# Kernel optimization log

Measured on AMD Instinct MI355X. Metric: run time of the kernel, lower is better.

Reference implementation:

```python
import jax, jax.numpy as jnp
import numpy as np

INPUT_LENGTH = 4096
NUM_FEATURES = 10000
KERNEL_LENGTH = 9
NUM_KERNELS = 84
EPS = 1e-12


def _compute_dilations(input_length):
    # mirrors MiniRocketTransform._compute_dilations exactly
    max_dilation = (input_length - 1) // (KERNEL_LENGTH - 1)
    dilations = np.logspace(0, np.log10(max_dilation), num=NUM_KERNELS, base=2, dtype=int)
    return np.unique(dilations).tolist()

DILATIONS = _compute_dilations(INPUT_LENGTH)  # static python ints


def _generate_kernels(seed=42):
    # mirrors MiniRocketTransform._generate_kernels; kernels with sum==0 dropped
    rng = np.random.RandomState(seed)
    ks = []
    for _ in range(NUM_KERNELS):
        k = rng.choice([-1, 2], size=KERNEL_LENGTH, p=[2.0 / 3.0, 1.0 / 3.0])
        if k.sum() != 0:
            ks.append(k)
    return np.asarray(ks, dtype=np.float32)


def setup_inputs() -> dict:
    key = jax.random.key(0)
    x = jax.random.normal(key, (256, 1, INPUT_LENGTH), dtype=jnp.float32)
    kernels = jnp.asarray(_generate_kernels())  # (Kn, 9)
    return {"x": x, "kernels": kernels}


def reference(x, kernels):
    # x: (B, 1, L); kernels: (Kn, 9) of {-1, 2}
    B = x.shape[0]
    w = kernels[:, None, :]  # (Kn, 1, 9) OIH

    # zero-stuffed dilated kernel + padding=0 (len((1,1,K) tensor)//2 == 0)
    # is exactly a VALID conv with rhs_dilation=d.
    def conv(xv, wv, d):
        return jax.lax.conv_general_dilated(
            xv, wv, window_strides=(1,), padding='VALID', rhs_dilation=(d,))

    # biases computed ONCE from the first kernel / first dilation conv output
    conv0 = conv(x, w[:1], DILATIONS[0])  # (B, 1, L0)
    q = jnp.quantile(conv0, jnp.array([0.25, 0.5, 0.75], dtype=conv0.dtype), axis=2)  # (3, B, 1)
    biases = q.mean(axis=1).reshape(3)  # (3,)

    feats = []
    for d in DILATIONS:  # small static set (~6)
        c = conv(x, w, d)  # (B, Kn, Ld)
        # PPV: fraction of positions where conv output exceeds each bias
        ppv = (c[:, :, None, :] > biases[None, None, :, None]).astype(jnp.float32).mean(axis=3)  # (B, Kn, 3)
        feats.append(ppv)

    # feature order in torch: kernel-major, then dilation, then bias
    f = jnp.stack(feats, axis=2).reshape(B, -1)  # (B, Kn*Dn*3)
    out = jnp.zeros((B, NUM_FEATURES), dtype=jnp.float32).at[:, :f.shape[1]].set(f)
    # F.normalize(p=2, dim=-1, eps=1e-12)
    norm = jnp.maximum(jnp.linalg.norm(out, axis=-1, keepdims=True), EPS)
    return out / norm
```

## Files before the change

kernel.cpp:

```cpp
#include <hip/hip_runtime.h>
#include <stdint.h>

#define IN_LEN 4096
#define NFEAT  10000

__device__ __forceinline__ void count_gt_f32(unsigned& cnt, float thr, float val) {
  asm volatile("v_cmp_lt_f32 vcc, %1, %2\n\t"
               "v_addc_co_u32 %0, vcc, 0, %0, vcc"
               : "+v"(cnt)
               : "v"(thr), "v"(val)
               : "vcc");
}
__device__ __forceinline__ void count_le_u32(unsigned& cnt, unsigned mid, unsigned key) {
  asm volatile("v_cmp_ge_u32 vcc, %1, %2\n\t"
               "v_addc_co_u32 %0, vcc, 0, %0, vcc"
               : "+v"(cnt)
               : "v"(mid), "v"(key)
               : "vcc");
}

__device__ __forceinline__ unsigned key_of(float f) {
  unsigned u = __float_as_uint(f);
  return (u & 0x80000000u) ? ~u : (u | 0x80000000u);
}
__device__ __forceinline__ float key_inv(unsigned k) {
  unsigned u = (k & 0x80000000u) ? (k ^ 0x80000000u) : ~k;
  return __uint_as_float(u);
}

__global__ __launch_bounds__(256) void quant_kernel(const float* __restrict__ x,
                                                    const float* __restrict__ kern,
                                                    float* __restrict__ ws_q) {
  const int b = blockIdx.x, tid = threadIdx.x;
  __shared__ __align__(16) float xs[IN_LEN];
  __shared__ unsigned redc[2][3 * 4];

  const float4* xg = (const float4*)(x + (size_t)b * IN_LEN);
  float4* xs4 = (float4*)xs;
  for (int i = tid; i < IN_LEN / 4; i += 256) xs4[i] = xg[i];

  float w[9];
#pragma unroll
  for (int j = 0; j < 9; j++) w[j] = kern[j];
  __syncthreads();

  const int L = IN_LEN - 8;
  unsigned keys[16];
#pragma unroll
  for (int i = 0; i < 16; i++) {
    int t = tid + (i << 8);
    if (t < L) {
      float c = 0.f;
#pragma unroll
      for (int j = 0; j < 9; j++) c = fmaf(w[j], xs[t + j], c);
      keys[i] = key_of(c);
    } else {
      keys[i] = 0xFFFFFFFFu;
    }
  }

  const int targ[6] = {1021, 1022, 2043, 2044, 3065, 3066};
  unsigned lo[6], hi[6];
#pragma unroll
  for (int q = 0; q < 6; q++) { lo[q] = 0u; hi[q] = 0xFFFFFFFFu; }

  const int wave = tid >> 6, lane = tid & 63;
  for (int it = 0; it < 32; ++it) {
    const int buf = it & 1;
    unsigned mid[6], cnt[6];
#pragma unroll
    for (int q = 0; q < 6; q++) { mid[q] = lo[q] + ((hi[q] - lo[q]) >> 1); cnt[q] = 0u; }
#pragma unroll
    for (int i = 0; i < 16; i++)
#pragma unroll
      for (int q = 0; q < 6; q++) count_le_u32(cnt[q], mid[q], keys[i]);
    unsigned r[3];
#pragma unroll
    for (int q = 0; q < 3; q++) r[q] = cnt[2 * q] | (cnt[2 * q + 1] << 16);
#pragma unroll
    for (int q = 0; q < 3; q++) {
#pragma unroll
      for (int off = 32; off > 0; off >>= 1) r[q] += (unsigned)__shfl_xor((int)r[q], off);
    }
    if (lane == 0) {
#pragma unroll
      for (int q = 0; q < 3; q++) redc[buf][q * 4 + wave] = r[q];
    }
    __syncthreads();
#pragma unroll
    for (int q = 0; q < 3; q++) {
      unsigned tot = redc[buf][q * 4 + 0] + redc[buf][q * 4 + 1] +
                     redc[buf][q * 4 + 2] + redc[buf][q * 4 + 3];
      unsigned t0 = tot & 0xFFFFu, t1 = tot >> 16;
      if (t0 >= (unsigned)(targ[2 * q] + 1)) hi[2 * q] = mid[2 * q]; else lo[2 * q] = mid[2 * q] + 1;
      if (t1 >= (unsigned)(targ[2 * q + 1] + 1)) hi[2 * q + 1] = mid[2 * q + 1]; else lo[2 * q + 1] = mid[2 * q + 1] + 1;
    }
  }

  if (tid == 0) {
    float v[6];
#pragma unroll
    for (int q = 0; q < 6; q++) v[q] = key_inv(lo[q]);
    ws_q[b * 3 + 0] = v[0] + 0.75f * (v[1] - v[0]);
    ws_q[b * 3 + 1] = v[2] + 0.5f  * (v[3] - v[2]);
    ws_q[b * 3 + 2] = v[4] + 0.25f * (v[5] - v[4]);
  }
}

__global__ __launch_bounds__(256) void bias_kernel(const float* __restrict__ ws_q,
                                                   float* __restrict__ ws_bias, int B) {
  __shared__ float red[256];
  const int tid = threadIdx.x;
  for (int q = 0; q < 3; q++) {
    float v = 0.f;
    for (int i = tid; i < B; i += 256) v += ws_q[i * 3 + q];
    red[tid] = v;
    __syncthreads();
    for (int s = 128; s > 0; s >>= 1) {
      if (tid < s) red[tid] += red[tid + s];
      __syncthreads();
    }
    if (tid == 0) ws_bias[q] = red[0] / (float)B;
    __syncthreads();
  }
}

template <int D>
__device__ __forceinline__ void run_feat(const float* xs,
                                         const float* __restrict__ kern,
                                         float b0, float b1, float b2,
                                         float* __restrict__ out, int K, int b) {
  const int tid = threadIdx.x;
  const int wave = tid >> 6, lane = tid & 63;
  constexpr int L = IN_LEN - 8 * D;
  constexpr int NFULL = 31;
  constexpr int KT = 8;

  const int KPW = (K + 3) >> 2;
  const int kstart = wave * KPW;
  const int kend = (kstart + KPW < K) ? (kstart + KPW) : K;

  for (int k0 = kstart; k0 < kend; k0 += KT) {
    float w[KT][9];
#pragma unroll
    for (int kk = 0; kk < KT; kk++) {
      const int kidx = (k0 + kk < K) ? (k0 + kk) : (K - 1);
      const bool ok = (k0 + kk) < kend;
      const float* wp = kern + (size_t)kidx * 9;
#pragma unroll
      for (int j = 0; j < 9; j++) w[kk][j] = ok ? wp[j] : 0.f;
    }
    unsigned c0[KT], c1[KT], c2[KT];
#pragma unroll
    for (int kk = 0; kk < KT; kk++) { c0[kk] = 0u; c1[kk] = 0u; c2[kk] = 0u; }

#pragma unroll 1
    for (int p = 0; p < NFULL; ++p) {
      const int t = (p << 7) + lane;
      float tax[9], tay[9];
#pragma unroll
      for (int j = 0; j < 9; j++) {
        tax[j] = xs[t + j * D];
        tay[j] = xs[t + 64 + j * D];
      }
#pragma unroll
      for (int kk = 0; kk < KT; kk++) {
        float ca = 0.f, cb = 0.f;
#pragma unroll
        for (int j = 0; j < 9; j++) {
          ca = fmaf(w[kk][j], tax[j], ca);
          cb = fmaf(w[kk][j], tay[j], cb);
        }
        count_gt_f32(c0[kk], b0, ca); count_gt_f32(c0[kk], b0, cb);
        count_gt_f32(c1[kk], b1, ca); count_gt_f32(c1[kk], b1, cb);
        count_gt_f32(c2[kk], b2, ca); count_gt_f32(c2[kk], b2, cb);
      }
    }
    {
      const int t = (NFULL << 7) + lane;
      const bool v0 = t < L, v1 = (t + 64) < L;
      float tax[9], tay[9];
#pragma unroll
      for (int j = 0; j < 9; j++) {
        tax[j] = xs[t + j * D];
        tay[j] = xs[t + 64 + j * D];
      }
#pragma unroll
      for (int kk = 0; kk < KT; kk++) {
        float ca = 0.f, cb = 0.f;
#pragma unroll
        for (int j = 0; j < 9; j++) {
          ca = fmaf(w[kk][j], tax[j], ca);
          cb = fmaf(w[kk][j], tay[j], cb);
        }
        ca = v0 ? ca : -3.0e38f;
        cb = v1 ? cb : -3.0e38f;
        count_gt_f32(c0[kk], b0, ca); count_gt_f32(c0[kk], b0, cb);
        count_gt_f32(c1[kk], b1, ca); count_gt_f32(c1[kk], b1, cb);
        count_gt_f32(c2[kk], b2, ca); count_gt_f32(c2[kk], b2, cb);
      }
    }

#pragma unroll
    for (int kk = 0; kk < KT; kk++) {
      unsigned r0 = c0[kk] | (c2[kk] << 16);
      unsigned r1 = c1[kk];
#pragma unroll
      for (int off = 32; off > 0; off >>= 1) {
        r0 += (unsigned)__shfl_xor((int)r0, off);
        r1 += (unsigned)__shfl_xor((int)r1, off);
      }
      const int k = k0 + kk;
      if (lane == 0 && k < kend) {
        float* o = out + (size_t)b * NFEAT + (size_t)k * 18 + (D - 1) * 3;
        o[0] = (float)(r0 & 0xFFFFu) / (float)L;
        o[1] = (float)r1 / (float)L;
        o[2] = (float)(r0 >> 16) / (float)L;
      }
    }
  }
}

__global__ __launch_bounds__(256) void feat_kernel(const float* __restrict__ x,
                                                   const float* __restrict__ kern,
                                                   const float* __restrict__ ws_bias,
                                                   float* __restrict__ out, int K) {
  __shared__ __align__(16) float xs[IN_LEN + 48];
  const int b = blockIdx.y, tid = threadIdx.x;

  const float4* xg = (const float4*)(x + (size_t)b * IN_LEN);
  float4* xs4 = (float4*)xs;
  for (int i = tid; i < IN_LEN / 4; i += 256) xs4[i] = xg[i];
  if (tid < 48) xs[IN_LEN + tid] = 0.f;
  const float b0 = ws_bias[0], b1 = ws_bias[1], b2 = ws_bias[2];
  __syncthreads();

  switch (blockIdx.x) {
    case 0: run_feat<1>(xs, kern, b0, b1, b2, out, K, b); break;
    case 1: run_feat<2>(xs, kern, b0, b1, b2, out, K, b); break;
    case 2: run_feat<3>(xs, kern, b0, b1, b2, out, K, b); break;
    case 3: run_feat<4>(xs, kern, b0, b1, b2, out, K, b); break;
    case 4: run_feat<5>(xs, kern, b0, b1, b2, out, K, b); break;
    case 5: run_feat<6>(xs, kern, b0, b1, b2, out, K, b); break;
  }
}

__global__ __launch_bounds__(256) void norm_kernel(float* __restrict__ out, int F) {
  const int b = blockIdx.x, tid = threadIdx.x;
  __shared__ float red[256];
  float acc = 0.f;
  for (int i = tid; i < F; i += 256) {
    float v = out[(size_t)b * NFEAT + i];
    acc = fmaf(v, v, acc);
  }
  red[tid] = acc;
  __syncthreads();
  for (int s = 128; s > 0; s >>= 1) {
    if (tid < s) red[tid] += red[tid + s];
    __syncthreads();
  }
  const float inv = 1.0f / fmaxf(sqrtf(red[0]), 1e-12f);
  for (int i = tid; i < F; i += 256) out[(size_t)b * NFEAT + i] *= inv;
}

extern "C" void kernel_launch(void* const* d_in, const int* in_sizes, int n_in,
                              void* d_out, int out_size, void* d_ws, size_t ws_size,
                              hipStream_t stream) {
  const float* x = (const float*)d_in[0];
  const float* kern = (const float*)d_in[1];
  float* out = (float*)d_out;
  const int B = in_sizes[0] / IN_LEN;
  const int K = in_sizes[1] / 9;

  float* ws_q = (float*)d_ws;
  float* ws_bias = ws_q + B * 3;

  hipMemsetAsync(d_out, 0, (size_t)out_size * sizeof(float), stream);

  quant_kernel<<<B, 256, 0, stream>>>(x, kern, ws_q);
  bias_kernel<<<1, 256, 0, stream>>>(ws_q, ws_bias, B);
  dim3 g(6, B);
  feat_kernel<<<g, 256, 0, stream>>>(x, kern, ws_bias, out, K);
  norm_kernel<<<B, 256, 0, stream>>>(out, K * 18);
}
```

Baseline: 231.2 us.

## Fuse bias and norm into producer kernels via last-block atomics, bitmask counting

Merges the bias reduction into the quantile kernel and the L2 normalization into the feature kernel, using atomic last-block-done counters. This removes two launches and the full-output memset, since the norm pass now writes the zero padding itself. Threshold comparisons are packed into bitmasks with alignbit on the sign of (bias - conv) and counted with popcount, with K tile reduced from 8 to 6 and an occupancy hint added. The atomic counters need a small workspace memset each call, and the sign-bit test differs from a strict greater-than when the difference is exactly zero.

```diff
diff --git a/kernel.cpp b/kernel.cpp
--- a/kernel.cpp
+++ b/kernel.cpp
@@ -4,19 +4,17 @@
 #define IN_LEN 4096
 #define NFEAT  10000
 
-__device__ __forceinline__ void count_gt_f32(unsigned& cnt, float thr, float val) {
-  asm volatile("v_cmp_lt_f32 vcc, %1, %2\n\t"
-               "v_addc_co_u32 %0, vcc, 0, %0, vcc"
-               : "+v"(cnt)
-               : "v"(thr), "v"(val)
-               : "vcc");
-}
-__device__ __forceinline__ void count_le_u32(unsigned& cnt, unsigned mid, unsigned key) {
-  asm volatile("v_cmp_ge_u32 vcc, %1, %2\n\t"
-               "v_addc_co_u32 %0, vcc, 0, %0, vcc"
-               : "+v"(cnt)
-               : "v"(mid), "v"(key)
-               : "vcc");
+#define WS_CNTA 0
+#define WS_DONE 256
+#define WS_Q    2048
+#define WS_BIAS 8192
+
+__device__ __forceinline__ void count_le_u32(unsigned& cnt, unsigned long long& cc,
+                                             unsigned mid, unsigned key) {
+  asm("v_cmp_ge_u32 %[cc], %[m], %[k]\n\t"
+      "v_addc_co_u32 %[c], %[cc], 0, %[c], %[cc]"
+      : [c] "+v"(cnt), [cc] "=&s"(cc)
+      : [m] "s"(mid), [k] "v"(key));
 }
 
 __device__ __forceinline__ unsigned key_of(float f) {
@@ -28,12 +26,18 @@
   return __uint_as_float(u);
 }
 
-__global__ __launch_bounds__(256) void quant_kernel(const float* __restrict__ x,
-                                                    const float* __restrict__ kern,
-                                                    float* __restrict__ ws_q) {
+__global__ __launch_bounds__(256) void quantbias_kernel(const float* __restrict__ x,
+                                                        const float* __restrict__ kern,
+                                                        unsigned char* __restrict__ ws) {
   const int b = blockIdx.x, tid = threadIdx.x;
+  float* ws_q = (float*)(ws + WS_Q);
+  float* ws_bias = (float*)(ws + WS_BIAS);
+  unsigned* cntA = (unsigned*)(ws + WS_CNTA);
+
   __shared__ __align__(16) float xs[IN_LEN];
   __shared__ unsigned redc[2][3 * 4];
+  __shared__ float redm[256];
+  __shared__ unsigned lastflag;
 
   const float4* xg = (const float4*)(x + (size_t)b * IN_LEN);
   float4* xs4 = (float4*)xs;
@@ -68,12 +72,13 @@
   for (int it = 0; it < 32; ++it) {
     const int buf = it & 1;
     unsigned mid[6], cnt[6];
+    unsigned long long ccq[3];
 #pragma unroll
     for (int q = 0; q < 6; q++) { mid[q] = lo[q] + ((hi[q] - lo[q]) >> 1); cnt[q] = 0u; }
 #pragma unroll
     for (int i = 0; i < 16; i++)
 #pragma unroll
-      for (int q = 0; q < 6; q++) count_le_u32(cnt[q], mid[q], keys[i]);
+      for (int q = 0; q < 6; q++) count_le_u32(cnt[q], ccq[q >> 1], mid[q], keys[i]);
     unsigned r[3];
 #pragma unroll
     for (int q = 0; q < 3; q++) r[q] = cnt[2 * q] | (cnt[2 * q + 1] << 16);
@@ -105,22 +110,27 @@
     ws_q[b * 3 + 1] = v[2] + 0.5f  * (v[3] - v[2]);
     ws_q[b * 3 + 2] = v[4] + 0.25f * (v[5] - v[4]);
   }
-}
-
-__global__ __launch_bounds__(256) void bias_kernel(const float* __restrict__ ws_q,
-                                                   float* __restrict__ ws_bias, int B) {
-  __shared__ float red[256];
-  const int tid = threadIdx.x;
+
+  __syncthreads();
+  if (tid == 0) {
+    __threadfence();
+    unsigned old = __hip_atomic_fetch_add(cntA, 1u, __ATOMIC_ACQ_REL, __HIP_MEMORY_SCOPE_AGENT);
+    lastflag = (old == gridDim.x - 1) ? 1u : 0u;
+  }
+  __syncthreads();
+  if (lastflag == 0u) return;
+  __threadfence();
+  const int B = gridDim.x;
   for (int q = 0; q < 3; q++) {
     float v = 0.f;
     for (int i = tid; i < B; i += 256) v += ws_q[i * 3 + q];
-    red[tid] = v;
+    redm[tid] = v;
     __syncthreads();
     for (int s = 128; s > 0; s >>= 1) {
-      if (tid < s) red[tid] += red[tid + s];
+      if (tid < s) redm[tid] += redm[tid + s];
       __syncthreads();
     }
-    if (tid == 0) ws_bias[q] = red[0] / (float)B;
+    if (tid == 0) ws_bias[q] = redm[0] / (float)B;
     __syncthreads();
   }
 }
@@ -129,12 +139,11 @@
 __device__ __forceinline__ void run_feat(const float* xs,
                                          const float* __restrict__ kern,
                                          float b0, float b1, float b2,
-                                         float* __restrict__ out, int K, int b) {
+                                         float* __restrict__ row, int K) {
   const int tid = threadIdx.x;
   const int wave = tid >> 6, lane = tid & 63;
   constexpr int L = IN_LEN - 8 * D;
-  constexpr int NFULL = 31;
-  constexpr int KT = 8;
+  constexpr int KT = 6;
 
   const int KPW = (K + 3) >> 2;
   const int kstart = wave * KPW;
@@ -151,18 +160,19 @@
       for (int j = 0; j < 9; j++) w[kk][j] = ok ? wp[j] : 0.f;
     }
     unsigned c0[KT], c1[KT], c2[KT];
-#pragma unroll
-    for (int kk = 0; kk < KT; kk++) { c0[kk] = 0u; c1[kk] = 0u; c2[kk] = 0u; }
+    unsigned m0[KT], m1[KT], m2[KT];
+#pragma unroll
+    for (int kk = 0; kk < KT; kk++) {
+      c0[kk] = 0u; c1[kk] = 0u; c2[kk] = 0u;
+      m0[kk] = 0u; m1[kk] = 0u; m2[kk] = 0u;
+    }
 
 #pragma unroll 1
-    for (int p = 0; p < NFULL; ++p) {
+    for (int p = 0; p < 16; ++p) {
       const int t = (p << 7) + lane;
       float tax[9], tay[9];
 #pragma unroll
-      for (int j = 0; j < 9; j++) {
-        tax[j] = xs[t + j * D];
-        tay[j] = xs[t + 64 + j * D];
-      }
+      for (int j = 0; j < 9; j++) { tax[j] = xs[t + j * D]; tay[j] = xs[t + 64 + j * D]; }
 #pragma unroll
       for (int kk = 0; kk < KT; kk++) {
         float ca = 0.f, cb = 0.f;
@@ -171,20 +181,27 @@
           ca = fmaf(w[kk][j], tax[j], ca);
           cb = fmaf(w[kk][j], tay[j], cb);
         }
-        count_gt_f32(c0[kk], b0, ca); count_gt_f32(c0[kk], b0, cb);
-        count_gt_f32(c1[kk], b1, ca); count_gt_f32(c1[kk], b1, cb);
-        count_gt_f32(c2[kk], b2, ca); count_gt_f32(c2[kk], b2, cb);
-      }
-    }
-    {
-      const int t = (NFULL << 7) + lane;
-      const bool v0 = t < L, v1 = (t + 64) < L;
+        m0[kk] = __builtin_amdgcn_alignbit(m0[kk], __float_as_uint(b0 - ca), 31);
+        m0[kk] = __builtin_amdgcn_alignbit(m0[kk], __float_as_uint(b0 - cb), 31);
+        m1[kk] = __builtin_amdgcn_alignbit(m1[kk], __float_as_uint(b1 - ca), 31);
+        m1[kk] = __builtin_amdgcn_alignbit(m1[kk], __float_as_uint(b1 - cb), 31);
+        m2[kk] = __builtin_amdgcn_alignbit(m2[kk], __float_as_uint(b2 - ca), 31);
+        m2[kk] = __builtin_amdgcn_alignbit(m2[kk], __float_as_uint(b2 - cb), 31);
+      }
+    }
+#pragma unroll
+    for (int kk = 0; kk < KT; kk++) {
+      c0[kk] += (unsigned)__popc(m0[kk]); m0[kk] = 0u;
+      c1[kk] += (unsigned)__popc(m1[kk]); m1[kk] = 0u;
+      c2[kk] += (unsigned)__popc(m2[kk]); m2[kk] = 0u;
+    }
+
+#pragma unroll 1
+    for (int p = 16; p < 31; ++p) {
+      const int t = (p << 7) + lane;
       float tax[9], tay[9];
 #pragma unroll
-      for (int j = 0; j < 9; j++) {
-        tax[j] = xs[t + j * D];
-        tay[j] = xs[t + 64 + j * D];
-      }
+      for (int j = 0; j < 9; j++) { tax[j] = xs[t + j * D]; tay[j] = xs[t + 64 + j * D]; }
 #pragma unroll
       for (int kk = 0; kk < KT; kk++) {
         float ca = 0.f, cb = 0.f;
@@ -193,12 +210,42 @@
           ca = fmaf(w[kk][j], tax[j], ca);
           cb = fmaf(w[kk][j], tay[j], cb);
         }
-        ca = v0 ? ca : -3.0e38f;
+        m0[kk] = __builtin_amdgcn_alignbit(m0[kk], __float_as_uint(b0 - ca), 31);
+        m0[kk] = __builtin_amdgcn_alignbit(m0[kk], __float_as_uint(b0 - cb), 31);
+        m1[kk] = __builtin_amdgcn_alignbit(m1[kk], __float_as_uint(b1 - ca), 31);
+        m1[kk] = __builtin_amdgcn_alignbit(m1[kk], __float_as_uint(b1 - cb), 31);
+        m2[kk] = __builtin_amdgcn_alignbit(m2[kk], __float_as_uint(b2 - ca), 31);
+        m2[kk] = __builtin_amdgcn_alignbit(m2[kk], __float_as_uint(b2 - cb), 31);
+      }
+    }
+    {
+      const int t = 3968 + lane;
+      const bool v1 = (t + 64) < L;
+      float tax[9], tay[9];
+#pragma unroll
+      for (int j = 0; j < 9; j++) { tax[j] = xs[t + j * D]; tay[j] = xs[t + 64 + j * D]; }
+#pragma unroll
+      for (int kk = 0; kk < KT; kk++) {
+        float ca = 0.f, cb = 0.f;
+#pragma unroll
+        for (int j = 0; j < 9; j++) {
+          ca = fmaf(w[kk][j], tax[j], ca);
+          cb = fmaf(w[kk][j], tay[j], cb);
+        }
         cb = v1 ? cb : -3.0e38f;
-        count_gt_f32(c0[kk], b0, ca); count_gt_f32(c0[kk], b0, cb);
-        count_gt_f32(c1[kk], b1, ca); count_gt_f32(c1[kk], b1, cb);
-        count_gt_f32(c2[kk], b2, ca); count_gt_f32(c2[kk], b2, cb);
-      }
+        m0[kk] = __builtin_amdgcn_alignbit(m0[kk], __float_as_uint(b0 - ca), 31);
+        m0[kk] = __builtin_amdgcn_alignbit(m0[kk], __float_as_uint(b0 - cb), 31);
+        m1[kk] = __builtin_amdgcn_alignbit(m1[kk], __float_as_uint(b1 - ca), 31);
+        m1[kk] = __builtin_amdgcn_alignbit(m1[kk], __float_as_uint(b1 - cb), 31);
+        m2[kk] = __builtin_amdgcn_alignbit(m2[kk], __float_as_uint(b2 - ca), 31);
+        m2[kk] = __builtin_amdgcn_alignbit(m2[kk], __float_as_uint(b2 - cb), 31);
+      }
+    }
+#pragma unroll
+    for (int kk = 0; kk < KT; kk++) {
+      c0[kk] += (unsigned)__popc(m0[kk]);
+      c1[kk] += (unsigned)__popc(m1[kk]);
+      c2[kk] += (unsigned)__popc(m2[kk]);
     }
 
 #pragma unroll
@@ -212,7 +259,7 @@
       }
       const int k = k0 + kk;
       if (lane == 0 && k < kend) {
-        float* o = out + (size_t)b * NFEAT + (size_t)k * 18 + (D - 1) * 3;
+        float* o = row + (size_t)k * 18 + (D - 1) * 3;
         o[0] = (float)(r0 & 0xFFFFu) / (float)L;
         o[1] = (float)r1 / (float)L;
         o[2] = (float)(r0 >> 16) / (float)L;
@@ -221,12 +268,16 @@
   }
 }
 
-__global__ __launch_bounds__(256) void feat_kernel(const float* __restrict__ x,
-                                                   const float* __restrict__ kern,
-                                                   const float* __restrict__ ws_bias,
-                                                   float* __restrict__ out, int K) {
+__global__ __launch_bounds__(256, 6) void feat_norm_kernel(const float* __restrict__ x,
+                                                           const float* __restrict__ kern,
+                                                           unsigned char* __restrict__ ws,
+                                                           float* __restrict__ out, int K) {
   __shared__ __align__(16) float xs[IN_LEN + 48];
+  __shared__ float red[256];
+  __shared__ unsigned lastflag;
   const int b = blockIdx.y, tid = threadIdx.x;
+  const float* ws_bias = (const float*)(ws + WS_BIAS);
+  unsigned* done = (unsigned*)(ws + WS_DONE);
 
   const float4* xg = (const float4*)(x + (size_t)b * IN_LEN);
   float4* xs4 = (float4*)xs;
@@ -235,22 +286,30 @@
   const float b0 = ws_bias[0], b1 = ws_bias[1], b2 = ws_bias[2];
   __syncthreads();
 
+  float* row = out + (size_t)b * NFEAT;
   switch (blockIdx.x) {
-    case 0: run_feat<1>(xs, kern, b0, b1, b2, out, K, b); break;
-    case 1: run_feat<2>(xs, kern, b0, b1, b2, out, K, b); break;
-    case 2: run_feat<3>(xs, kern, b0, b1, b2, out, K, b); break;
-    case 3: run_feat<4>(xs, kern, b0, b1, b2, out, K, b); break;
-    case 4: run_feat<5>(xs, kern, b0, b1, b2, out, K, b); break;
-    case 5: run_feat<6>(xs, kern, b0, b1, b2, out, K, b); break;
-  }
-}
-
-__global__ __launch_bounds__(256) void norm_kernel(float* __restrict__ out, int F) {
-  const int b = blockIdx.x, tid = threadIdx.x;
-  __shared__ float red[256];
+    case 0: run_feat<1>(xs, kern, b0, b1, b2, row, K); break;
+    case 1: run_feat<2>(xs, kern, b0, b1, b2, row, K); break;
+    case 2: run_feat<3>(xs, kern, b0, b1, b2, row, K); break;
+    case 3: run_feat<4>(xs, kern, b0, b1, b2, row, K); break;
+    case 4: run_feat<5>(xs, kern, b0, b1, b2, row, K); break;
+    case 5: run_feat<6>(xs, kern, b0, b1, b2, row, K); break;
+  }
+
+  __syncthreads();
+  if (tid == 0) {
+    __threadfence();
+    unsigned old = __hip_atomic_fetch_add(&done[b], 1u, __ATOMIC_ACQ_REL, __HIP_MEMORY_SCOPE_AGENT);
+    lastflag = (old == 5u) ? 1u : 0u;
+  }
+  __syncthreads();
+  if (lastflag == 0u) return;
+  __threadfence();
+
+  const int F = K * 18;
   float acc = 0.f;
   for (int i = tid; i < F; i += 256) {
-    float v = out[(size_t)b * NFEAT + i];
+    float v = row[i];
     acc = fmaf(v, v, acc);
   }
   red[tid] = acc;
@@ -260,7 +319,10 @@
     __syncthreads();
   }
   const float inv = 1.0f / fmaxf(sqrtf(red[0]), 1e-12f);
-  for (int i = tid; i < F; i += 256) out[(size_t)b * NFEAT + i] *= inv;
+  for (int i = tid; i < NFEAT; i += 256) {
+    float v = (i < F) ? row[i] * inv : 0.f;
+    row[i] = v;
+  }
 }
 
 extern "C" void kernel_launch(void* const* d_in, const int* in_sizes, int n_in,
@@ -271,15 +333,10 @@
   float* out = (float*)d_out;
   const int B = in_sizes[0] / IN_LEN;
   const int K = in_sizes[1] / 9;
-
-  float* ws_q = (float*)d_ws;
-  float* ws_bias = ws_q + B * 3;
-
-  hipMemsetAsync(d_out, 0, (size_t)out_size * sizeof(float), stream);
-
-  quant_kernel<<<B, 256, 0, stream>>>(x, kern, ws_q);
-  bias_kernel<<<1, 256, 0, stream>>>(ws_q, ws_bias, B);
+  unsigned char* ws = (unsigned char*)d_ws;
+
+  hipMemsetAsync(ws, 0, 2048, stream);
+  quantbias_kernel<<<B, 256, 0, stream>>>(x, kern, ws);
   dim3 g(6, B);
-  feat_kernel<<<g, 256, 0, stream>>>(x, kern, ws_bias, out, K);
-  norm_kernel<<<B, 256, 0, stream>>>(out, K * 18);
-}
+  feat_norm_kernel<<<g, 256, 0, stream>>>(x, kern, ws, out, K);
+}
```

Result: slower. 884.0 us (+282.4%).
